# Kernel tuning notes

Measured on AMD Instinct MI355X. Metric: run time of the kernel, lower is better.

## Reference

```python
import jax, jax.numpy as jnp
import numpy as np

N = 2_000_000   # total flattened logits (anchors x classes scale)
FG = 256        # number of foreground (targets==1) entries
DELTA = 1.0


def setup_inputs() -> dict:
    key = jax.random.key(0)
    k1, k2 = jax.random.split(key)
    logits = jax.random.normal(k1, (N,), dtype=jnp.float32)
    fg_idx = jax.random.choice(k2, N, shape=(FG,), replace=False)
    targets = jnp.zeros((N,), dtype=jnp.int32).at[fg_idx].set(1)
    return {"logits": logits, "targets": targets, "fg_num": FG}


def _ap_loss(logits, targets, fg_num):
    """Faithful port of AP_loss: returns (loss [1], grad [N]).

    The torch validity filter (targets==0 & logits >= min(fg)-delta) is
    redundant: for invalid bg, (l - fg_i)/(2*delta)+0.5 < 0, so clamp gives 0.
    We therefore mask with (targets==0) over the full array (static shapes).
    """
    bg_mask = (targets == 0).astype(logits.dtype)
    fg_idx = jnp.nonzero(targets == 1, size=fg_num)[0]
    fg_logits = logits[fg_idx]            # [fg]
    order = jnp.argsort(fg_logits)
    sorted_fg = fg_logits[order]          # ascending, matches torch loop order

    inv2d = 1.0 / (2.0 * DELTA)

    def step(carry, f_i):
        max_prec, bg_grad = carry
        tmp1 = jnp.clip((fg_logits - f_i) * inv2d + 0.5, 0.0, 1.0)   # [fg]
        tmp2 = jnp.clip((logits - f_i) * inv2d + 0.5, 0.0, 1.0) * bg_mask  # [N]
        a = jnp.sum(tmp1) + 0.5
        b = jnp.sum(tmp2)
        cur = a / (a + b)
        new_max = jnp.maximum(max_prec, cur)
        scale = jnp.where(max_prec <= cur, 1.0, (1.0 - max_prec) / (1.0 - cur))
        bg_grad = bg_grad + tmp2 * (scale / (a + b))
        return (new_max, bg_grad), new_max

    init = (jnp.zeros((), logits.dtype), jnp.zeros_like(logits))
    (_, bg_grad), prec_sorted = jax.lax.scan(step, init, sorted_fg)

    prec = jnp.zeros((fg_num,), logits.dtype).at[order].set(prec_sorted)
    grad = bg_grad.at[fg_idx].set(-(1.0 - prec))
    denom = max(fg_num, 1)
    grad = grad / denom
    metric = jnp.sum(prec, keepdims=True) / denom   # [1]
    return 1.0 - metric, grad


def reference(logits, targets, fg_num):
    loss, _ = _ap_loss(logits, targets, fg_num)
    return loss
```

## Files before the change

kernel.cpp:

```cpp
#include <hip/hip_runtime.h>

#define FG    256
#define NBIN  1024
#define BINV  32.0f
#define BOFF  512.0f

typedef unsigned long long u64;
typedef unsigned int u32;


__global__ void init_kernel(int* counter, u64* gacc) {
    int tid = threadIdx.x;
    if (tid == 0) *counter = 0;
    gacc[tid] = 0ull;
}

__global__ void __launch_bounds__(1024) hist_kernel(
        const float* __restrict__ logits,
        const int* __restrict__ targets,
        int* __restrict__ counter,
        float* __restrict__ fgraw,
        u64* __restrict__ gacc, int n) {
    __shared__ u32 h[NBIN];
    const int tid = threadIdx.x;
    h[tid] = 0u;
    __syncthreads();

    const int n4 = n >> 2;
    const float4* l4 = (const float4*)logits;
    const int4*   t4 = (const int4*)targets;
    const int stride = gridDim.x * blockDim.x;
    for (int i = blockIdx.x * blockDim.x + tid; i < n4; i += stride) {
        float4 x = l4[i];
        int4   t = t4[i];
        #pragma unroll
        for (int e = 0; e < 4; ++e) {
            float l  = (e == 0) ? x.x : (e == 1) ? x.y : (e == 2) ? x.z : x.w;
            int   tg = (e == 0) ? t.x : (e == 1) ? t.y : (e == 2) ? t.z : t.w;
            float u = fmaf(l, BINV, BOFF);
            u = fminf(fmaxf(u, 0.f), 1023.99f);
            int b = (int)u;
            u32 qoff = (u32)((u - (float)b) * 32.0f);
            atomicAdd(&h[b], (1u << 18) | qoff);
            if (tg == 1) {
                int p = atomicAdd(counter, 1);
                fgraw[p] = l;
            }
        }
    }
    if (blockIdx.x == 0 && tid == 0) {
        for (int i = n4 << 2; i < n; ++i) {
            float l = logits[i];
            float u = fmaf(l, BINV, BOFF);
            u = fminf(fmaxf(u, 0.f), 1023.99f);
            int b = (int)u;
            u32 qoff = (u32)((u - (float)b) * 32.0f);
            atomicAdd(&h[b], (1u << 18) | qoff);
            if (targets[i] == 1) { int p = atomicAdd(counter, 1); fgraw[p] = l; }
        }
    }
    __syncthreads();
    u32 v = h[tid];
    if (v) {
        u64 pk = ((u64)(v >> 18) << 32) | (u64)(v & 0x3FFFFu);
        atomicAdd(&gacc[tid], pk);
    }
}

__global__ void __launch_bounds__(1024) final_kernel(
        const float* __restrict__ fgraw,
        const u64* __restrict__ gacc,
        float* __restrict__ out, int n) {
    __shared__ float rc[NBIN], rs[NBIN];
    __shared__ float pc[NBIN], ps[NBIN];
    __shared__ float sfv[FG], sf[FG];
    __shared__ int   pr[1024];
    __shared__ float pa[1024];
    __shared__ float wc[16], ws[16];
    __shared__ float wm[4], wsum[4];
    const int tid  = threadIdx.x;
    const int lane = tid & 63;
    const int wv   = tid >> 6;

    {
        u64 v = gacc[tid];
        float cnt = (float)(u32)(v >> 32);
        float qs  = (float)(u32)(v & 0xFFFFFFFFull);
        float binlo = ((float)tid - BOFF) * (1.0f / BINV);
        rc[tid] = cnt;
        rs[tid] = fmaf(qs + 0.5f * cnt, 1.0f / 1024.0f, binlo * cnt);
    }
    if (tid < FG) sfv[tid] = fgraw[tid];
    __syncthreads();

    float c = rc[tid], s = rs[tid];
    #pragma unroll
    for (int off = 1; off < 64; off <<= 1) {
        float tc = __shfl_up(c, off, 64), ts = __shfl_up(s, off, 64);
        if (lane >= off) { c += tc; s += ts; }
    }
    if (lane == 63) { wc[wv] = c; ws[wv] = s; }

    {
        int i = tid & 255, ch = tid >> 8;
        float v = sfv[i];
        int r = 0;
        #pragma unroll 8
        for (int j = ch * 64; j < ch * 64 + 64; ++j) {
            float o = sfv[j];
            r += (o < v || (o == v && j < i)) ? 1 : 0;
        }
        pr[tid] = r;
    }
    __syncthreads();

    if (wv == 0 && lane < 16) {
        float cc = wc[lane], ss = ws[lane];
        #pragma unroll
        for (int off = 1; off < 16; off <<= 1) {
            float tc = __shfl_up(cc, off, 64), ts = __shfl_up(ss, off, 64);
            if (lane >= off) { cc += tc; ss += ts; }
        }
        wc[lane] = cc; ws[lane] = ss;
    }
    if (tid < FG) {
        int r = pr[tid] + pr[tid + 256] + pr[tid + 512] + pr[tid + 768];
        sf[r] = sfv[tid];
    }
    __syncthreads();
    if (wv > 0) { c += wc[wv - 1]; s += ws[wv - 1]; }
    pc[tid] = c; ps[tid] = s;

    {
        int i = tid & 255, ch = tid >> 8;
        float fi = sf[i];
        float sum = 0.f;
        #pragma unroll 8
        for (int j = ch * 64; j < ch * 64 + 64; ++j) {
            float v = (sf[j] - fi) * 0.5f + 0.5f;
            sum += fminf(fmaxf(v, 0.f), 1.f);
        }
        pa[tid] = sum;
    }
    __syncthreads();

    float cur = 0.f;
    if (tid < FG) {
        const float fi = sf[tid];
        const float a = 0.5f + pa[tid] + pa[tid + 256] + pa[tid + 512] + pa[tid + 768];
        float C[2], S[2];
        #pragma unroll
        for (int q = 0; q < 2; ++q) {
            float t = (q == 0) ? (fi - 1.0f) : (fi + 1.0f);
            float u = fmaf(t, BINV, BOFF);
            u = fminf(fmaxf(u, 0.f), 1023.99f);
            float kf = floorf(u);
            int   k  = (int)kf;
            float frac = u - kf;
            C[q] = pc[k] + rc[k] * (frac - 1.0f);
            S[q] = ps[k] + rs[k] * (frac - 1.0f);
        }
        const float Cab   = (float)n - C[1];
        const float Cw    = C[1] - C[0];
        const float Sw    = S[1] - S[0];
        const float b_all = Cab + 0.5f * Sw + (0.5f - 0.5f * fi) * Cw;
        const float b_bg  = b_all - (a - 0.5f);
        cur = a / (a + b_bg);
        float m = cur;
        #pragma unroll
        for (int off = 1; off < 64; off <<= 1) {
            float t = __shfl_up(m, off, 64);
            if (lane >= off) m = fmaxf(m, t);
        }
        if (lane == 63) wm[wv] = m;
        pr[tid] = __float_as_int(m);
    }
    __syncthreads();
    if (tid < FG) {
        float m = __int_as_float(pr[tid]);
        float pmax = -1.f;
        for (int w = 0; w < 4; ++w) if (w < wv) pmax = fmaxf(pmax, wm[w]);
        m = fmaxf(m, pmax);
        float v = m;
        #pragma unroll
        for (int off = 32; off; off >>= 1) v += __shfl_down(v, off, 64);
        if (lane == 0) wsum[wv] = v;
    }
    __syncthreads();
    if (tid == 0) {
        float t = (wsum[0] + wsum[1]) + (wsum[2] + wsum[3]);
        out[0] = 1.f - t / (float)FG;
    }
}

extern "C" void kernel_launch(void* const* d_in, const int* in_sizes, int n_in,
                              void* d_out, int out_size, void* d_ws, size_t ws_size,
                              hipStream_t stream) {
    const float* logits  = (const float*)d_in[0];
    const int*   targets = (const int*)d_in[1];
    const int n = in_sizes[0];

    char*  wb      = (char*)d_ws;
    int*   counter = (int*)wb;
    float* fgraw   = (float*)(wb + 256);
    u64*   gacc    = (u64*)(wb + 2048);
    float* out     = (float*)d_out;

    init_kernel<<<1, NBIN, 0, stream>>>(counter, gacc);
    hist_kernel<<<256, 1024, 0, stream>>>(logits, targets, counter, fgraw, gacc, n);
    final_kernel<<<1, NBIN, 0, stream>>>(fgraw, gacc, out, n);
}
```

Baseline: 79.66 us.

## Replace global atomics with per-block partial histograms and drop init kernel

New measurement: 85.91 us. 1.08x slower.

```diff
diff --git a/kernel.cpp b/kernel.cpp
--- a/kernel.cpp
+++ b/kernel.cpp
@@ -4,26 +4,24 @@
 #define NBIN  1024
 #define BINV  32.0f
 #define BOFF  512.0f
+#define NBLK  256
 
 typedef unsigned long long u64;
 typedef unsigned int u32;
 
-
-__global__ void init_kernel(int* counter, u64* gacc) {
-    int tid = threadIdx.x;
-    if (tid == 0) *counter = 0;
-    gacc[tid] = 0ull;
-}
 
 __global__ void __launch_bounds__(1024) hist_kernel(
         const float* __restrict__ logits,
         const int* __restrict__ targets,
-        int* __restrict__ counter,
-        float* __restrict__ fgraw,
-        u64* __restrict__ gacc, int n) {
+        float* __restrict__ fgslots,
+        int* __restrict__ fgcnt,
+        u32* __restrict__ partials, int n) {
     __shared__ u32 h[NBIN];
+    __shared__ float lfg[FG];
+    __shared__ int lcnt;
     const int tid = threadIdx.x;
     h[tid] = 0u;
+    if (tid == 0) lcnt = 0;
     __syncthreads();
 
     const int n4 = n >> 2;
@@ -43,8 +41,8 @@
             u32 qoff = (u32)((u - (float)b) * 32.0f);
             atomicAdd(&h[b], (1u << 18) | qoff);
             if (tg == 1) {
-                int p = atomicAdd(counter, 1);
-                fgraw[p] = l;
+                int p = atomicAdd(&lcnt, 1);
+                if (p < FG) lfg[p] = l;
             }
         }
     }
@@ -56,20 +54,23 @@
             int b = (int)u;
             u32 qoff = (u32)((u - (float)b) * 32.0f);
             atomicAdd(&h[b], (1u << 18) | qoff);
-            if (targets[i] == 1) { int p = atomicAdd(counter, 1); fgraw[p] = l; }
-        }
-    }
-    __syncthreads();
-    u32 v = h[tid];
-    if (v) {
-        u64 pk = ((u64)(v >> 18) << 32) | (u64)(v & 0x3FFFFu);
-        atomicAdd(&gacc[tid], pk);
-    }
+            if (targets[i] == 1) {
+                int p = atomicAdd(&lcnt, 1);
+                if (p < FG) lfg[p] = l;
+            }
+        }
+    }
+    __syncthreads();
+    partials[blockIdx.x * NBIN + tid] = h[tid];
+    const int c = (lcnt < FG) ? lcnt : FG;
+    if (tid == 0) fgcnt[blockIdx.x] = c;
+    if (tid < c) fgslots[blockIdx.x * FG + tid] = lfg[tid];
 }
 
 __global__ void __launch_bounds__(1024) final_kernel(
-        const float* __restrict__ fgraw,
-        const u64* __restrict__ gacc,
+        const int* __restrict__ fgcnt,
+        const float* __restrict__ fgslots,
+        const u32* __restrict__ partials,
         float* __restrict__ out, int n) {
     __shared__ float rc[NBIN], rs[NBIN];
     __shared__ float pc[NBIN], ps[NBIN];
@@ -78,19 +79,56 @@
     __shared__ float pa[1024];
     __shared__ float wc[16], ws[16];
     __shared__ float wm[4], wsum[4];
+    __shared__ u32   ucnt[NBIN], uqs[NBIN];
+    __shared__ int   fwp[4];
     const int tid  = threadIdx.x;
     const int lane = tid & 63;
     const int wv   = tid >> 6;
 
-    {
-        u64 v = gacc[tid];
-        float cnt = (float)(u32)(v >> 32);
-        float qs  = (float)(u32)(v & 0xFFFFFFFFull);
+    ucnt[tid] = 0u; uqs[tid] = 0u;
+    int fv = (tid < FG) ? fgcnt[tid] : 0;
+    __syncthreads();
+
+    {
+        const uint4* p4 = (const uint4*)partials;
+        u32 c0=0,c1=0,c2=0,c3=0,q0=0,q1=0,q2=0,q3=0;
+        #pragma unroll 8
+        for (int k = 0; k < 64; ++k) {
+            uint4 v = p4[tid + (k << 10)];
+            c0 += v.x >> 18; q0 += v.x & 0x3FFFFu;
+            c1 += v.y >> 18; q1 += v.y & 0x3FFFFu;
+            c2 += v.z >> 18; q2 += v.z & 0x3FFFFu;
+            c3 += v.w >> 18; q3 += v.w & 0x3FFFFu;
+        }
+        const int bb = (tid & 255) << 2;
+        atomicAdd(&ucnt[bb + 0], c0); atomicAdd(&uqs[bb + 0], q0);
+        atomicAdd(&ucnt[bb + 1], c1); atomicAdd(&uqs[bb + 1], q1);
+        atomicAdd(&ucnt[bb + 2], c2); atomicAdd(&uqs[bb + 2], q2);
+        atomicAdd(&ucnt[bb + 3], c3); atomicAdd(&uqs[bb + 3], q3);
+    }
+    int fs = fv;
+    if (tid < FG) {
+        #pragma unroll
+        for (int off = 1; off < 64; off <<= 1) {
+            int t = __shfl_up(fs, off, 64);
+            if (lane >= off) fs += t;
+        }
+        if (lane == 63) fwp[wv] = fs;
+    }
+    __syncthreads();
+
+    {
+        float cnt = (float)ucnt[tid];
+        float qs  = (float)uqs[tid];
         float binlo = ((float)tid - BOFF) * (1.0f / BINV);
         rc[tid] = cnt;
         rs[tid] = fmaf(qs + 0.5f * cnt, 1.0f / 1024.0f, binlo * cnt);
     }
-    if (tid < FG) sfv[tid] = fgraw[tid];
+    if (tid < FG) {
+        int excl = fs - fv;
+        for (int w = 0; w < wv; ++w) excl += fwp[w];
+        for (int j = 0; j < fv; ++j) sfv[excl + j] = fgslots[tid * FG + j];
+    }
     __syncthreads();
 
     float c = rc[tid], s = rs[tid];
@@ -200,13 +238,12 @@
     const int*   targets = (const int*)d_in[1];
     const int n = in_sizes[0];
 
-    char*  wb      = (char*)d_ws;
-    int*   counter = (int*)wb;
-    float* fgraw   = (float*)(wb + 256);
-    u64*   gacc    = (u64*)(wb + 2048);
-    float* out     = (float*)d_out;
-
-    init_kernel<<<1, NBIN, 0, stream>>>(counter, gacc);
-    hist_kernel<<<256, 1024, 0, stream>>>(logits, targets, counter, fgraw, gacc, n);
-    final_kernel<<<1, NBIN, 0, stream>>>(fgraw, gacc, out, n);
+    char*  wb       = (char*)d_ws;
+    int*   fgcnt    = (int*)wb;
+    float* fgslots  = (float*)(wb + 4096);
+    u32*   partials = (u32*)(wb + (1 << 20));
+    float* out      = (float*)d_out;
+
+    hist_kernel<<<NBLK, 1024, 0, stream>>>(logits, targets, fgslots, fgcnt, partials, n);
+    final_kernel<<<1, 1024, 0, stream>>>(fgcnt, fgslots, partials, out, n);
 }
```
